# Kernel optimization log

Hardware: AMD Instinct MI355X
Metric: run time of the kernel (lower is better)

## Reference

```python
import jax, jax.numpy as jnp
import numpy as np
from jax import lax

H = 256       # hidden_size (hard-coded via .view(256,1) in source)
V = 10000     # vocab
NOPS = 9      # ops: 0 sum, 1 count, 2 diff, 3 greater, 4 lesser, 5 and, 6 or, 7 assign, 8 reset
COLS = 64
ROWS = 200000
T = 4         # num_time_steps
QLEN = 40
NNUM = 5


def setup_inputs() -> dict:
    key = jax.random.key(0)
    ks = jax.random.split(key, 16)
    s = 0.02
    return {
        'input_question': jax.random.randint(ks[0], (QLEN,), 0, V),
        'question_numbers': jax.random.normal(ks[1], (NNUM,), jnp.float32),
        'left_word_indices': jax.random.randint(ks[2], (NNUM,), 0, QLEN),
        'table': jax.random.normal(ks[3], (ROWS, COLS), jnp.float32),
        # question RNN params
        'E': jax.random.normal(ks[4], (V, H), jnp.float32) * s,
        'Wx': jax.random.normal(ks[5], (H, H), jnp.float32) * s,
        'Wh': jax.random.normal(ks[6], (H, H), jnp.float32) * s,
        'b': jnp.zeros((H,), jnp.float32),
        # selector params
        'W_op': jax.random.normal(ks[7], (H, 2 * H), jnp.float32) * s,
        'op_emb': jax.random.normal(ks[8], (NOPS, H), jnp.float32) * s,
        'W_col': jax.random.normal(ks[9], (H, 2 * H), jnp.float32) * s,
        'col_emb': jax.random.normal(ks[10], (COLS, H), jnp.float32) * s,
        # pivot embeddings U(0)=lesser, U(1)=greater
        'U': jax.random.normal(ks[11], (2, H), jnp.float32) * s,
        # history RNN params
        'W_hc': jax.random.normal(ks[12], (H, 2 * H), jnp.float32) * s,
        'W_hh': jax.random.normal(ks[13], (H, H), jnp.float32) * s,
    }


def reference(input_question, question_numbers, left_word_indices, table,
              E, Wx, Wh, b, W_op, op_emb, W_col, col_emb, U, W_hc, W_hh):
    rows = table.shape[0]
    # ---- question RNN (simple tanh RNN over embedded words) ----
    x = E[input_question]                                  # [Q, H]
    def cell(h, xt):
        hn = jnp.tanh(xt @ Wx + h @ Wh + b)
        return hn, hn
    q, states = lax.scan(cell, jnp.zeros((H,), table.dtype), x)   # q: [H], states: [Q, H]
    Z = states[left_word_indices]                          # z_matrix [N, H]

    # ---- pivots (train mode: soft attention over question numbers) ----
    beta_l = jax.nn.softmax(Z @ U[0])                      # [N]
    beta_g = jax.nn.softmax(Z @ U[1])
    l_pivot = beta_l @ question_numbers                    # scalar
    g_pivot = beta_g @ question_numbers

    row_selects = [jnp.ones((rows,), table.dtype)]
    scalars = [jnp.zeros((), table.dtype)]
    h_hist = jnp.zeros((H,), table.dtype)
    lookup = jnp.zeros(table.shape, table.dtype)

    for t in range(T):
        qh = jnp.concatenate([q, h_hist])                  # [2H]
        a_op = jax.nn.softmax(op_emb @ jnp.tanh(W_op @ qh))    # [NOPS]
        a_col = jax.nn.softmax(col_emb @ jnp.tanh(W_col @ qh)) # [COLS]

        rs1 = row_selects[-1]
        rs2 = row_selects[max(0, len(row_selects) - 2)]
        s1 = scalars[-1]
        s3 = scalars[max(0, len(scalars) - 3)]

        col_val = table @ a_col                            # [R] column-weighted table values
        g_sel = (table > g_pivot).astype(table.dtype) @ a_col  # [R]
        l_sel = (table < l_pivot).astype(table.dtype) @ a_col

        row_select = (a_op[3] * g_sel + a_op[4] * l_sel
                      + a_op[5] * jnp.minimum(rs1, rs2)
                      + a_op[6] * jnp.maximum(rs1, rs2)
                      + a_op[8] * 1.0
                      + (a_op[0] + a_op[1] + a_op[2] + a_op[7]) * rs1)

        scalar = (a_op[0] * (rs1 @ col_val)
                  + a_op[1] * jnp.sum(rs1)
                  + a_op[2] * (s3 - s1))

        lookup = a_op[7] * row_select[:, None] * a_col[None, :]   # [R, C]

        c = jnp.concatenate([a_op @ op_emb, a_col @ col_emb])     # [2H]
        h_hist = jnp.tanh(W_hc @ c + W_hh @ h_hist)

        row_selects.append(row_select)
        scalars.append(scalar)

    return scalars[-1], lookup
```

## Files before the change

### kernel.cpp

```cpp
#include <hip/hip_runtime.h>
#include <math.h>

#define H 256
#define COLSN 64
#define ROWSN 200000
#define T_STEPS 4
#define QLEN 40
#define NNUM 5
#define NOPS 9

#define WS_UBUF   0
#define WS_HBUF   3072
#define WS_XWB    0
#define WS_Q      10240
#define WS_AOP    10496
#define WS_ACOL   10560
#define WS_PIV    10816
#define WS_TICKET 10818
#define WS_PACC8  10824
#define WS_EPOCH  10840
#define WS_ARR    10844
#define WS_MOP    11104
#define WS_MCOL   13408

#define NTBL_TILES  1563
#define NTBL_BLOCKS 782
#define NSEL_BLOCKS 13
#define NM_BLOCKS   72

template<int CTRL>
__device__ __forceinline__ float dpp_add(float x) {
    int xi = __float_as_int(x);
    int yi = __builtin_amdgcn_update_dpp(0, xi, CTRL, 0xF, 0xF, true);
    return x + __int_as_float(yi);
}
#define DPP_XOR1 0xB1
#define DPP_XOR2 0x4E
#define DPP_HMIR 0x141
#define DPP_MIR  0x140

__device__ __forceinline__ float reduce16(float v) {
    v = dpp_add<DPP_XOR1>(v);
    v = dpp_add<DPP_XOR2>(v);
    v = dpp_add<DPP_HMIR>(v);
    v = dpp_add<DPP_MIR>(v);
    return v;
}

__device__ __forceinline__ float fast_tanh(float x) {
    float cx = fminf(15.f, fmaxf(-15.f, x));
    float e = __expf(2.f * cx);
    return __fdividef(e - 1.f, e + 1.f);
}

__device__ __forceinline__ float dot4(float4 a, float4 b) {
    return a.x * b.x + a.y * b.y + a.z * b.z + a.w * b.w;
}

__device__ __forceinline__ float aread(float* p) { return atomicAdd(p, 0.f); }

__device__ __forceinline__ int sw(int i) { return i + ((i >> 4) << 2); }

__global__ __launch_bounds__(256) void k_pre(const int* __restrict__ iq,
        const float* __restrict__ E, const float* __restrict__ Wx,
        const float* __restrict__ b, const float* __restrict__ W_hc,
        const float* __restrict__ op_emb, const float* __restrict__ col_emb,
        float* __restrict__ ws) {
    int blk = blockIdx.x;
    int tid = threadIdx.x;
    if (blk < QLEN) {
        if (blk == 0 && tid < 32) ws[WS_TICKET + tid] = 0.f;
        int word = iq[blk];
        const float* erow = E + (long)word * H;
        float a0 = b[tid], a1 = 0.f, a2 = 0.f, a3 = 0.f;
        #pragma unroll 8
        for (int j = 0; j < H; j += 4) {
            a0 += erow[j + 0] * Wx[(j + 0) * H + tid];
            a1 += erow[j + 1] * Wx[(j + 1) * H + tid];
            a2 += erow[j + 2] * Wx[(j + 2) * H + tid];
            a3 += erow[j + 3] * Wx[(j + 3) * H + tid];
        }
        ws[WS_XWB + blk * H + tid] = (a0 + a1) + (a2 + a3);
    } else {
        __shared__ __attribute__((aligned(16))) float tile[32][268];
        int mb = blk - QLEN;
        int bi = mb / 9;
        int kg = mb % 9;
        int ibase = bi * 32;
        int coff = (kg == 0) ? 0 : H;
        for (int idx = tid; idx < 32 * 64; idx += 256) {
            int r = idx >> 6, c4 = idx & 63;
            float4 v = *(const float4*)&W_hc[(long)(ibase + r) * 2 * H + coff + c4 * 4];
            float* d = &tile[r][c4 * 4];
            d[0] = v.x; d[1] = v.y; d[2] = v.z; d[3] = v.w;
        }
        __syncthreads();
        int l8 = tid & 7;
        int io = tid >> 3;
        int nk = (kg == 0) ? NOPS : 8;
        for (int kk = 0; kk < nk; ++kk) {
            const float* emb;
            int dst;
            if (kg == 0) { emb = op_emb + kk * H;                 dst = WS_MOP + kk * H; }
            else { int c = (kg - 1) * 8 + kk; emb = col_emb + c * H; dst = WS_MCOL + c * H; }
            float s = 0.f;
            const float* ep = emb + l8 * 32;
            const float* tr = &tile[io][l8 * 32];
            #pragma unroll
            for (int ss = 0; ss < 8; ++ss) {
                int q4 = (ss + l8) & 7;
                float4 e4 = *(const float4*)&ep[q4 * 4];
                float4 t4 = *(const float4*)&tr[q4 * 4];
                s += dot4(e4, t4);
            }
            s += __shfl_xor(s, 1);
            s += __shfl_xor(s, 2);
            s += __shfl_xor(s, 4);
            if (l8 == 0) ws[dst + ibase + io] = s;
        }
    }
}

__global__ __launch_bounds__(1024) void k_rnn(const float* __restrict__ Wh,
                      const int* __restrict__ lwi,
                      const float* __restrict__ U, const float* __restrict__ qn,
                      float* __restrict__ ws) {
    __shared__ __attribute__((aligned(16))) float hbuf[2][288];
    __shared__ __attribute__((aligned(16))) float xwb[QLEN][H];
    __shared__ float Z[NNUM][H];
    __shared__ float lg[10];
    int tid = threadIdx.x;
    int g = tid >> 3;
    int p = tid & 7;

    float2 w2[32];
    #pragma unroll
    for (int jj = 0; jj < 32; ++jj)
        w2[jj] = *(const float2*)&Wh[(p * 32 + jj) * H + g * 2];

    {
        const float4* src = (const float4*)&ws[WS_XWB];
        float4* dst = (float4*)&xwb[0][0];
        for (int idx = tid; idx < QLEN * H / 4; idx += 1024) dst[idx] = src[idx];
    }
    if (tid < H) hbuf[0][tid + ((tid >> 5) << 2)] = 0.f;
    __syncthreads();

    int lw0 = lwi[0], lw1 = lwi[1], lw2 = lwi[2], lw3 = lwi[3], lw4 = lwi[4];
    int cur = 0;
    for (int t = 0; t < QLEN; ++t) {
        const float4* hv = (const float4*)&hbuf[cur][p * 36];
        float a0 = 0.f, a1 = 0.f;
        #pragma unroll
        for (int q4 = 0; q4 < 8; ++q4) {
            float4 h4 = hv[q4];
            float2 wa = w2[q4 * 4 + 0];
            float2 wb = w2[q4 * 4 + 1];
            float2 wc = w2[q4 * 4 + 2];
            float2 wd = w2[q4 * 4 + 3];
            a0 += h4.x * wa.x; a1 += h4.x * wa.y;
            a0 += h4.y * wb.x; a1 += h4.y * wb.y;
            a0 += h4.z * wc.x; a1 += h4.z * wc.y;
            a0 += h4.w * wd.x; a1 += h4.w * wd.y;
        }
        a0 = dpp_add<DPP_XOR1>(a0); a0 = dpp_add<DPP_XOR2>(a0); a0 = dpp_add<DPP_HMIR>(a0);
        a1 = dpp_add<DPP_XOR1>(a1); a1 = dpp_add<DPP_XOR2>(a1); a1 = dpp_add<DPP_HMIR>(a1);
        if (p < 2) {
            float s = (p == 0) ? a0 : a1;
            int i = g * 2 + p;
            float hn = fast_tanh(xwb[t][i] + s);
            hbuf[cur ^ 1][i + ((i >> 5) << 2)] = hn;
            if (t == lw0) Z[0][i] = hn;
            if (t == lw1) Z[1][i] = hn;
            if (t == lw2) Z[2][i] = hn;
            if (t == lw3) Z[3][i] = hn;
            if (t == lw4) Z[4][i] = hn;
        }
        __syncthreads();
        cur ^= 1;
    }
    if (tid < H) ws[WS_Q + tid] = hbuf[cur][tid + ((tid >> 5) << 2)];

    int grp = tid >> 5;
    int lane = tid & 31;
    if (grp < 10) {
        int u = grp / 5, n = grp % 5;
        float s = 0.f;
        #pragma unroll
        for (int k = 0; k < 8; ++k) {
            int j = lane + k * 32;
            s += Z[n][j] * U[u * H + j];
        }
        s += __shfl_xor(s, 1);
        s += __shfl_xor(s, 2);
        s += __shfl_xor(s, 4);
        s += __shfl_xor(s, 8);
        s += __shfl_xor(s, 16);
        if (lane == 0) lg[grp] = s;
    }
    __syncthreads();
    if (tid < 2) {
        float m = -1e30f;
        for (int n = 0; n < 5; ++n) m = fmaxf(m, lg[tid * 5 + n]);
        float e[5], s = 0.f;
        for (int n = 0; n < 5; ++n) { e[n] = expf(lg[tid * 5 + n] - m); s += e[n]; }
        float piv = 0.f;
        for (int n = 0; n < 5; ++n) piv += (e[n] / s) * qn[n];
        ws[WS_PIV + (tid == 0 ? 1 : 0)] = piv;
    }
    for (int i = tid; i < 4096; i += 1024) ws[WS_UBUF + i] = 0.f;
}

__global__ __launch_bounds__(256) void k_sel(
        const float* __restrict__ W_op, const float* __restrict__ W_col,
        const float* __restrict__ W_hh, const float* __restrict__ op_emb,
        const float* __restrict__ col_emb, float* __restrict__ ws) {
    const int tid = threadIdx.x;
    const int blk = blockIdx.x;

    if (blk == 0) {
        __shared__ float mopL[NOPS][H];
        __shared__ float mcolL[COLSN][H];
        __shared__ __attribute__((aligned(16))) float uopsw[320];
        __shared__ __attribute__((aligned(16))) float ucolsw[320];
        __shared__ float vhhL[H];
        __shared__ float lgs[80];
        __shared__ float aop_s[16], acol_s[64];

        for (int idx = tid; idx < (NOPS + COLSN) * H; idx += 256) {
            int row = idx >> 8, col = idx & 255;
            if (row < NOPS) mopL[row][col] = ws[WS_MOP + row * H + col];
            else            mcolL[row - NOPS][col] = ws[WS_MCOL + (row - NOPS) * H + col];
        }
        __syncthreads();

        for (int t = 0; t < T_STEPS; ++t) {
            if (tid == 0) {
                while (aread(&ws[WS_ARR + t]) < 11.5f) __builtin_amdgcn_s_sleep(16);
            }
            __syncthreads();
            float uo = aread(&ws[WS_UBUF + t * 768 + tid]);
            float uc = aread(&ws[WS_UBUF + t * 768 + 256 + tid]);
            float vh = aread(&ws[WS_UBUF + t * 768 + 512 + tid]);
            uopsw[sw(tid)] = uo;
            ucolsw[sw(tid)] = uc;
            vhhL[tid] = vh;
            __syncthreads();
            {
                int g = tid >> 4, p = tid & 15;
                int pb = p * 20;
                float4 uc0 = *(const float4*)&ucolsw[pb + 0];
                float4 uc1 = *(const float4*)&ucolsw[pb + 4];
                float4 uc2 = *(const float4*)&ucolsw[pb + 8];
                float4 uc3 = *(const float4*)&ucolsw[pb + 12];
                #pragma unroll
                for (int k = 0; k < 4; ++k) {
                    int o = g + k * 16;
                    const float* row = &col_emb[o * H + p * 16];
                    float4 e0 = *(const float4*)&row[0];
                    float4 e1 = *(const float4*)&row[4];
                    float4 e2 = *(const float4*)&row[8];
                    float4 e3 = *(const float4*)&row[12];
                    float s = dot4(e0, uc0) + dot4(e1, uc1) + dot4(e2, uc2) + dot4(e3, uc3);
                    s = reduce16(s);
                    if (p == 0) lgs[NOPS + o] = s;
                }
                if (g < NOPS) {
                    float4 uo0 = *(const float4*)&uopsw[pb + 0];
                    float4 uo1 = *(const float4*)&uopsw[pb + 4];
                    float4 uo2 = *(const float4*)&uopsw[pb + 8];
                    float4 uo3 = *(const float4*)&uopsw[pb + 12];
                    const float* row = &op_emb[g * H + p * 16];
                    float4 e0 = *(const float4*)&row[0];
                    float4 e1 = *(const float4*)&row[4];
                    float4 e2 = *(const float4*)&row[8];
                    float4 e3 = *(const float4*)&row[12];
                    float s = dot4(e0, uo0) + dot4(e1, uo1) + dot4(e2, uo2) + dot4(e3, uo3);
                    s = reduce16(s);
                    if (p == 0) lgs[g] = s;
                }
            }
            __syncthreads();
            if (tid == 0) {
                float m = -1e30f;
                for (int k = 0; k < NOPS; ++k) m = fmaxf(m, lgs[k]);
                float e[NOPS], s = 0.f;
                for (int k = 0; k < NOPS; ++k) { e[k] = expf(lgs[k] - m); s += e[k]; }
                float inv = 1.f / s;
                for (int k = 0; k < NOPS; ++k) {
                    float a = e[k] * inv;
                    aop_s[k] = a;
                    ws[WS_AOP + t * 16 + k] = a;
                }
            }
            if (tid >= 64 && tid < 128) {
                int lane = tid - 64;
                float v = lgs[NOPS + lane];
                float m = v;
                for (int off = 1; off < 64; off <<= 1) m = fmaxf(m, __shfl_xor(m, off));
                float e = expf(v - m);
                float s = e;
                for (int off = 1; off < 64; off <<= 1) s += __shfl_xor(s, off);
                float a = __fdividef(e, s);
                acol_s[lane] = a;
                ws[WS_ACOL + t * COLSN + lane] = a;
            }
            __syncthreads();
            if (t < T_STEPS - 1) {
                float s = vhhL[tid];
                #pragma unroll
                for (int k = 0; k < NOPS; ++k) s += aop_s[k] * mopL[k][tid];
                #pragma unroll 8
                for (int c = 0; c < COLSN; ++c) s += acol_s[c] * mcolL[c][tid];
                float hn = fast_tanh(s);
                atomicAdd(&ws[WS_HBUF + (t + 1) * 256 + tid], hn);
                __threadfence();
                __syncthreads();
                if (tid == 0) atomicAdd(&ws[WS_EPOCH], 1.f);
            }
        }
    } else {
        __shared__ float wlds[64 * 257];
        __shared__ float hl[H];
        __shared__ float Pl[64];
        __shared__ float pp[4][64];
        const int wb = (blk - 1) * 64;

        for (int idx = tid; idx < 64 * 64; idx += 256) {
            int r = idx >> 6, j4 = idx & 63;
            int o = wb + r;
            const float* src = (o < 256) ? &W_op[(long)o * 2 * H + H]
                             : (o < 512) ? &W_col[(long)(o - 256) * 2 * H + H]
                             : &W_hh[(long)(o - 512) * H];
            float4 v = *(const float4*)&src[j4 * 4];
            float* d = &wlds[r * 257 + j4 * 4];
            d[0] = v.x; d[1] = v.y; d[2] = v.z; d[3] = v.w;
        }
        hl[tid] = ws[WS_Q + tid];
        __syncthreads();
        {
            int r = tid >> 2, c = tid & 3;
            int o = wb + r;
            if (o < 512) {
                const float* src = (o < 256) ? &W_op[(long)o * 2 * H]
                                             : &W_col[(long)(o - 256) * 2 * H];
                const float* qq = &hl[c * 64];
                float s = 0.f;
                #pragma unroll
                for (int k = 0; k < 16; ++k) {
                    float4 w = *(const float4*)&src[c * 64 + k * 4];
                    s += w.x * qq[k*4] + w.y * qq[k*4+1] + w.z * qq[k*4+2] + w.w * qq[k*4+3];
                }
                s += __shfl_xor(s, 1);
                s += __shfl_xor(s, 2);
                if (c == 0) Pl[r] = s;
            } else if (c == 0) Pl[r] = 0.f;
        }
        __syncthreads();

        const int lane = tid & 63;
        const int seg = tid >> 6;
        for (int t = 0; t < T_STEPS; ++t) {
            if (t > 0) {
                if (tid == 0) {
                    while (aread(&ws[WS_EPOCH]) < (float)t - 0.5f) __builtin_amdgcn_s_sleep(16);
                }
                __syncthreads();
                hl[tid] = aread(&ws[WS_HBUF + t * 256 + tid]);
                __syncthreads();
            }
            float s = 0.f;
            if (t > 0) {
                const float* wr = &wlds[lane * 257 + seg * 64];
                const float* hh = &hl[seg * 64];
                #pragma unroll 8
                for (int j = 0; j < 64; ++j) s += wr[j] * hh[j];
            }
            pp[seg][lane] = s;
            __syncthreads();
            if (tid < 64) {
                float sum = pp[0][tid] + pp[1][tid] + pp[2][tid] + pp[3][tid];
                int o = wb + tid;
                float val = (o < 512) ? fast_tanh(Pl[tid] + sum) : sum;
                atomicAdd(&ws[WS_UBUF + t * 768 + o], val);
            }
            __threadfence();
            __syncthreads();
            if (tid == 0) atomicAdd(&ws[WS_ARR + t], 1.f);
            __syncthreads();
        }
    }
}

__global__ __launch_bounds__(512) void k_table(const float* __restrict__ table,
                                               float* __restrict__ ws,
                                               float* __restrict__ out) {
    __shared__ __attribute__((aligned(16))) float4 acT4[4][17];
    __shared__ float aop_l[64];
    __shared__ float rs3s[8][16];
    __shared__ float bred[8][8];
    __shared__ int lastblk;
    const int tid = threadIdx.x;
    const int wid = tid >> 6;
    const int lane = tid & 63;
    const int r16 = lane & 15;
    const int q = lane >> 4;

    if (tid < 64) {
        aop_l[tid] = ws[WS_AOP + tid];
        acT4[tid >> 4][tid & 15] = make_float4(
            ws[WS_ACOL + 0 * COLSN + tid], ws[WS_ACOL + 1 * COLSN + tid],
            ws[WS_ACOL + 2 * COLSN + tid], ws[WS_ACOL + 3 * COLSN + tid]);
    }
    __syncthreads();
    const float gp = ws[WS_PIV + 0];
    const float lp = ws[WS_PIV + 1];
    const float ac3 = acT4[q][r16].w;

    float dacc[4] = {0,0,0,0}, cacc[4] = {0,0,0,0};

    for (int tile = blockIdx.x; tile < NTBL_TILES; tile += NTBL_BLOCKS) {
        long wrow = (long)tile * 128 + wid * 16;
        bool active = wrow < ROWSN;

        float cv[4] = {0,0,0,0}, gs[4] = {0,0,0,0}, ls[4] = {0,0,0,0};
        if (active) {
            const float* src = table + (wrow + r16) * COLSN + q * 16;
            float4 x0 = *(const float4*)&src[0];
            float4 x1 = *(const float4*)&src[4];
            float4 x2 = *(const float4*)&src[8];
            float4 x3 = *(const float4*)&src[12];
            float xs[16] = {x0.x,x0.y,x0.z,x0.w, x1.x,x1.y,x1.z,x1.w,
                            x2.x,x2.y,x2.z,x2.w, x3.x,x3.y,x3.z,x3.w};
            #pragma unroll
            for (int jj = 0; jj < 16; ++jj) {
                float x = xs[jj];
                float4 a4 = acT4[q][jj];
                float gt = (x > gp) ? 1.f : 0.f;
                float lt = (x < lp) ? 1.f : 0.f;
                cv[0] += x * a4.x;  cv[1] += x * a4.y;  cv[2] += x * a4.z;  cv[3] += x * a4.w;
                gs[0] += gt * a4.x; gs[1] += gt * a4.y; gs[2] += gt * a4.z; gs[3] += gt * a4.w;
                ls[0] += lt * a4.x; ls[1] += lt * a4.y; ls[2] += lt * a4.z; ls[3] += lt * a4.w;
            }
        }
        #pragma unroll
        for (int k = 0; k < 4; ++k) {
            cv[k] += __shfl_xor(cv[k], 16); cv[k] += __shfl_xor(cv[k], 32);
            gs[k] += __shfl_xor(gs[k], 16); gs[k] += __shfl_xor(gs[k], 32);
            ls[k] += __shfl_xor(ls[k], 16); ls[k] += __shfl_xor(ls[k], 32);
        }

        float prev1 = 1.f, prev2 = 1.f;
        #pragma unroll
        for (int t = 0; t < 4; ++t) {
            if (active) { dacc[t] += prev1 * cv[t]; cacc[t] += prev1; }
            float cg = aop_l[t*16+3], cl = aop_l[t*16+4], cmn = aop_l[t*16+5];
            float cmx = aop_l[t*16+6], co = aop_l[t*16+8];
            float cid = aop_l[t*16+0] + aop_l[t*16+1] + aop_l[t*16+2] + aop_l[t*16+7];
            float rsn = cg * gs[t] + cl * ls[t] + cmn * fminf(prev1, prev2)
                      + cmx * fmaxf(prev1, prev2) + co + cid * prev1;
            prev2 = prev1; prev1 = rsn;
        }
        if (q == 0 && active) rs3s[wid][r16] = prev1 * aop_l[3*16+7];

        if (active) {
            float* dst = out + 1 + wrow * COLSN;
            #pragma unroll 4
            for (int s = 0; s < 16; ++s)
                dst[(long)s * COLSN + lane] = rs3s[wid][s] * ac3;
        }
    }

    float vals[8];
    #pragma unroll
    for (int t = 0; t < 4; ++t) { vals[t] = dacc[t]; vals[4 + t] = cacc[t]; }
    #pragma unroll
    for (int k = 0; k < 8; ++k) vals[k] = reduce16(vals[k]);
    if (lane == 0) {
        #pragma unroll
        for (int k = 0; k < 8; ++k) bred[wid][k] = vals[k];
    }
    __syncthreads();
    if (tid < 8) {
        float s = 0.f;
        #pragma unroll
        for (int w = 0; w < 8; ++w) s += bred[w][tid];
        atomicAdd(&ws[WS_PACC8 + tid], s);
    }
    __syncthreads();

    if (tid == 0) {
        float old = atomicAdd(&ws[WS_TICKET], 1.0f);
        lastblk = ((int)(old + 0.5f) == NTBL_BLOCKS - 1) ? 1 : 0;
    }
    __syncthreads();
    if (lastblk) {
        if (tid < 8) bred[0][tid] = atomicAdd(&ws[WS_PACC8 + tid], 0.f);
        __syncthreads();
        if (tid == 0) {
            float d0 = bred[0][0], d1 = bred[0][1], d2 = bred[0][2], d3 = bred[0][3];
            float c0 = bred[0][4], c1 = bred[0][5], c2 = bred[0][6], c3 = bred[0][7];
            float s0 = aop_l[0]*d0  + aop_l[1]*c0;
            float s1 = aop_l[16]*d1 + aop_l[17]*c1 + aop_l[18]*(0.f - s0);
            float s2 = aop_l[32]*d2 + aop_l[33]*c2 + aop_l[34]*(0.f - s1);
            float s3 = aop_l[48]*d3 + aop_l[49]*c3 + aop_l[50]*(s0 - s2);
            out[0] = s3;
        }
    }
}

extern "C" void kernel_launch(void* const* d_in, const int* in_sizes, int n_in,
                              void* d_out, int out_size, void* d_ws, size_t ws_size,
                              hipStream_t stream) {
    const int*   iq      = (const int*)  d_in[0];
    const float* qn      = (const float*)d_in[1];
    const int*   lwi     = (const int*)  d_in[2];
    const float* table   = (const float*)d_in[3];
    const float* E       = (const float*)d_in[4];
    const float* Wx      = (const float*)d_in[5];
    const float* Wh      = (const float*)d_in[6];
    const float* b       = (const float*)d_in[7];
    const float* W_op    = (const float*)d_in[8];
    const float* op_emb  = (const float*)d_in[9];
    const float* W_col   = (const float*)d_in[10];
    const float* col_emb = (const float*)d_in[11];
    const float* U       = (const float*)d_in[12];
    const float* W_hc    = (const float*)d_in[13];
    const float* W_hh    = (const float*)d_in[14];
    float* out = (float*)d_out;
    float* ws  = (float*)d_ws;

    hipLaunchKernelGGL(k_pre,  dim3(QLEN + NM_BLOCKS), dim3(256), 0, stream,
                       iq, E, Wx, b, W_hc, op_emb, col_emb, ws);
    hipLaunchKernelGGL(k_rnn,  dim3(1), dim3(1024), 0, stream, Wh, lwi, U, qn, ws);
    hipLaunchKernelGGL(k_sel,  dim3(NSEL_BLOCKS), dim3(256), 0, stream,
                       W_op, W_col, W_hh, op_emb, col_emb, ws);
    hipLaunchKernelGGL(k_table, dim3(NTBL_BLOCKS), dim3(512), 0, stream,
                       table, ws, out);
}
```

Measured before the change: 133.3 us.

## Fuse pre, RNN and selector kernels into one persistent kernel with flag sync

Replaces the separate k_pre, k_rnn and k_sel launches with a tiny zeroing kernel plus one fused 95-block kernel. Inside it, roles are assigned by block index and handed off through global atomic counters (XW done, M done, Q done). The history-RNN step is now computed redundantly in each of the 12 selector blocks from LDS-resident M matrices, which removes the single-block broadcast epoch round-trip. This targets launch gaps and the inter-block serialization per time step, at the cost of spin-wait dependencies that assume all blocks are co-resident, plus redundant compute.

```diff
diff --git a/kernel.cpp b/kernel.cpp
--- a/kernel.cpp
+++ b/kernel.cpp
@@ -10,7 +10,6 @@
 #define NOPS 9
 
 #define WS_UBUF   0
-#define WS_HBUF   3072
 #define WS_XWB    0
 #define WS_Q      10240
 #define WS_AOP    10496
@@ -18,15 +17,19 @@
 #define WS_PIV    10816
 #define WS_TICKET 10818
 #define WS_PACC8  10824
-#define WS_EPOCH  10840
-#define WS_ARR    10844
+#define WS_ARR    10832
+#define WS_XWDONE 10836
+#define WS_MDONE  10837
+#define WS_QDONE  10838
 #define WS_MOP    11104
 #define WS_MCOL   13408
 
 #define NTBL_TILES  1563
 #define NTBL_BLOCKS 782
-#define NSEL_BLOCKS 13
-#define NM_BLOCKS   72
+#define NW 12
+#define NXW 10
+#define NMB 72
+#define NFUSED (NW + 1 + NXW + NMB)
 
 template<int CTRL>
 __device__ __forceinline__ float dpp_add(float x) {
@@ -61,223 +64,122 @@
 
 __device__ __forceinline__ int sw(int i) { return i + ((i >> 4) << 2); }
 
-__global__ __launch_bounds__(256) void k_pre(const int* __restrict__ iq,
-        const float* __restrict__ E, const float* __restrict__ Wx,
-        const float* __restrict__ b, const float* __restrict__ W_hc,
+__global__ void k_zero(float* __restrict__ ws) {
+    int t = threadIdx.x;
+    if (t < 22) ws[WS_TICKET + t] = 0.f;
+}
+
+__global__ __launch_bounds__(1024) void k_fused(
+        const int* __restrict__ iq, const int* __restrict__ lwi,
+        const float* __restrict__ qn, const float* __restrict__ E,
+        const float* __restrict__ Wx, const float* __restrict__ b,
+        const float* __restrict__ Wh, const float* __restrict__ U,
+        const float* __restrict__ W_op, const float* __restrict__ W_col,
+        const float* __restrict__ W_hh, const float* __restrict__ W_hc,
         const float* __restrict__ op_emb, const float* __restrict__ col_emb,
         float* __restrict__ ws) {
-    int blk = blockIdx.x;
-    int tid = threadIdx.x;
-    if (blk < QLEN) {
-        if (blk == 0 && tid < 32) ws[WS_TICKET + tid] = 0.f;
-        int word = iq[blk];
-        const float* erow = E + (long)word * H;
-        float a0 = b[tid], a1 = 0.f, a2 = 0.f, a3 = 0.f;
-        #pragma unroll 8
-        for (int j = 0; j < H; j += 4) {
-            a0 += erow[j + 0] * Wx[(j + 0) * H + tid];
-            a1 += erow[j + 1] * Wx[(j + 1) * H + tid];
-            a2 += erow[j + 2] * Wx[(j + 2) * H + tid];
-            a3 += erow[j + 3] * Wx[(j + 3) * H + tid];
-        }
-        ws[WS_XWB + blk * H + tid] = (a0 + a1) + (a2 + a3);
-    } else {
-        __shared__ __attribute__((aligned(16))) float tile[32][268];
-        int mb = blk - QLEN;
-        int bi = mb / 9;
-        int kg = mb % 9;
-        int ibase = bi * 32;
-        int coff = (kg == 0) ? 0 : H;
-        for (int idx = tid; idx < 32 * 64; idx += 256) {
-            int r = idx >> 6, c4 = idx & 63;
-            float4 v = *(const float4*)&W_hc[(long)(ibase + r) * 2 * H + coff + c4 * 4];
-            float* d = &tile[r][c4 * 4];
-            d[0] = v.x; d[1] = v.y; d[2] = v.z; d[3] = v.w;
-        }
-        __syncthreads();
-        int l8 = tid & 7;
-        int io = tid >> 3;
-        int nk = (kg == 0) ? NOPS : 8;
-        for (int kk = 0; kk < nk; ++kk) {
-            const float* emb;
-            int dst;
-            if (kg == 0) { emb = op_emb + kk * H;                 dst = WS_MOP + kk * H; }
-            else { int c = (kg - 1) * 8 + kk; emb = col_emb + c * H; dst = WS_MCOL + c * H; }
-            float s = 0.f;
-            const float* ep = emb + l8 * 32;
-            const float* tr = &tile[io][l8 * 32];
-            #pragma unroll
-            for (int ss = 0; ss < 8; ++ss) {
-                int q4 = (ss + l8) & 7;
-                float4 e4 = *(const float4*)&ep[q4 * 4];
-                float4 t4 = *(const float4*)&tr[q4 * 4];
-                s += dot4(e4, t4);
-            }
-            s += __shfl_xor(s, 1);
-            s += __shfl_xor(s, 2);
-            s += __shfl_xor(s, 4);
-            if (l8 == 0) ws[dst + ibase + io] = s;
-        }
-    }
-}
-
-__global__ __launch_bounds__(1024) void k_rnn(const float* __restrict__ Wh,
-                      const int* __restrict__ lwi,
-                      const float* __restrict__ U, const float* __restrict__ qn,
-                      float* __restrict__ ws) {
-    __shared__ __attribute__((aligned(16))) float hbuf[2][288];
-    __shared__ __attribute__((aligned(16))) float xwb[QLEN][H];
-    __shared__ float Z[NNUM][H];
-    __shared__ float lg[10];
-    int tid = threadIdx.x;
-    int g = tid >> 3;
-    int p = tid & 7;
-
-    float2 w2[32];
-    #pragma unroll
-    for (int jj = 0; jj < 32; ++jj)
-        w2[jj] = *(const float2*)&Wh[(p * 32 + jj) * H + g * 2];
-
-    {
-        const float4* src = (const float4*)&ws[WS_XWB];
-        float4* dst = (float4*)&xwb[0][0];
-        for (int idx = tid; idx < QLEN * H / 4; idx += 1024) dst[idx] = src[idx];
-    }
-    if (tid < H) hbuf[0][tid + ((tid >> 5) << 2)] = 0.f;
-    __syncthreads();
-
-    int lw0 = lwi[0], lw1 = lwi[1], lw2 = lwi[2], lw3 = lwi[3], lw4 = lwi[4];
-    int cur = 0;
-    for (int t = 0; t < QLEN; ++t) {
-        const float4* hv = (const float4*)&hbuf[cur][p * 36];
-        float a0 = 0.f, a1 = 0.f;
-        #pragma unroll
-        for (int q4 = 0; q4 < 8; ++q4) {
-            float4 h4 = hv[q4];
-            float2 wa = w2[q4 * 4 + 0];
-            float2 wb = w2[q4 * 4 + 1];
-            float2 wc = w2[q4 * 4 + 2];
-            float2 wd = w2[q4 * 4 + 3];
-            a0 += h4.x * wa.x; a1 += h4.x * wa.y;
-            a0 += h4.y * wb.x; a1 += h4.y * wb.y;
-            a0 += h4.z * wc.x; a1 += h4.z * wc.y;
-            a0 += h4.w * wd.x; a1 += h4.w * wd.y;
-        }
-        a0 = dpp_add<DPP_XOR1>(a0); a0 = dpp_add<DPP_XOR2>(a0); a0 = dpp_add<DPP_HMIR>(a0);
-        a1 = dpp_add<DPP_XOR1>(a1); a1 = dpp_add<DPP_XOR2>(a1); a1 = dpp_add<DPP_HMIR>(a1);
-        if (p < 2) {
-            float s = (p == 0) ? a0 : a1;
-            int i = g * 2 + p;
-            float hn = fast_tanh(xwb[t][i] + s);
-            hbuf[cur ^ 1][i + ((i >> 5) << 2)] = hn;
-            if (t == lw0) Z[0][i] = hn;
-            if (t == lw1) Z[1][i] = hn;
-            if (t == lw2) Z[2][i] = hn;
-            if (t == lw3) Z[3][i] = hn;
-            if (t == lw4) Z[4][i] = hn;
-        }
-        __syncthreads();
-        cur ^= 1;
-    }
-    if (tid < H) ws[WS_Q + tid] = hbuf[cur][tid + ((tid >> 5) << 2)];
-
-    int grp = tid >> 5;
-    int lane = tid & 31;
-    if (grp < 10) {
-        int u = grp / 5, n = grp % 5;
-        float s = 0.f;
-        #pragma unroll
-        for (int k = 0; k < 8; ++k) {
-            int j = lane + k * 32;
-            s += Z[n][j] * U[u * H + j];
-        }
-        s += __shfl_xor(s, 1);
-        s += __shfl_xor(s, 2);
-        s += __shfl_xor(s, 4);
-        s += __shfl_xor(s, 8);
-        s += __shfl_xor(s, 16);
-        if (lane == 0) lg[grp] = s;
-    }
-    __syncthreads();
-    if (tid < 2) {
-        float m = -1e30f;
-        for (int n = 0; n < 5; ++n) m = fmaxf(m, lg[tid * 5 + n]);
-        float e[5], s = 0.f;
-        for (int n = 0; n < 5; ++n) { e[n] = expf(lg[tid * 5 + n] - m); s += e[n]; }
-        float piv = 0.f;
-        for (int n = 0; n < 5; ++n) piv += (e[n] / s) * qn[n];
-        ws[WS_PIV + (tid == 0 ? 1 : 0)] = piv;
-    }
-    for (int i = tid; i < 4096; i += 1024) ws[WS_UBUF + i] = 0.f;
-}
-
-__global__ __launch_bounds__(256) void k_sel(
-        const float* __restrict__ W_op, const float* __restrict__ W_col,
-        const float* __restrict__ W_hh, const float* __restrict__ op_emb,
-        const float* __restrict__ col_emb, float* __restrict__ ws) {
+    __shared__ __attribute__((aligned(16))) float smem[36864];
     const int tid = threadIdx.x;
     const int blk = blockIdx.x;
 
-    if (blk == 0) {
-        __shared__ float mopL[NOPS][H];
-        __shared__ float mcolL[COLSN][H];
-        __shared__ __attribute__((aligned(16))) float uopsw[320];
-        __shared__ __attribute__((aligned(16))) float ucolsw[320];
-        __shared__ float vhhL[H];
-        __shared__ float lgs[80];
-        __shared__ float aop_s[16], acol_s[64];
-
-        for (int idx = tid; idx < (NOPS + COLSN) * H; idx += 256) {
-            int row = idx >> 8, col = idx & 255;
-            if (row < NOPS) mopL[row][col] = ws[WS_MOP + row * H + col];
-            else            mcolL[row - NOPS][col] = ws[WS_MCOL + (row - NOPS) * H + col];
-        }
-        __syncthreads();
+    if (blk < NW) {
+        float* wlds  = smem;
+        float* mlds  = smem + 16448;
+        float* hl    = smem + 35136;
+        float* Pl    = smem + 35456;
+        float* uop   = smem + 35520;
+        float* ucol  = smem + 35840;
+        float* vhh   = smem + 36160;
+        float* lgs   = smem + 36416;
+        float* aop_s = smem + 36496;
+        float* acol_s= smem + 36512;
+        const int wb = blk * 64;
+        const int r  = tid >> 4;
+        const int p  = tid & 15;
+        const int pb = p * 20;
+
+        for (int idx = tid; idx < 64 * 64; idx += 1024) {
+            int rr = idx >> 6, j4 = idx & 63;
+            int o = wb + rr;
+            const float* src = (o < 256) ? &W_op[(long)o * 512 + 256]
+                             : (o < 512) ? &W_col[(long)(o - 256) * 512 + 256]
+                             : &W_hh[(long)(o - 512) * 256];
+            float4 v = *(const float4*)&src[j4 * 4];
+            float* d = &wlds[rr * 257 + j4 * 4];
+            d[0] = v.x; d[1] = v.y; d[2] = v.z; d[3] = v.w;
+        }
+        if (tid == 0) while (aread(&ws[WS_MDONE]) < NMB - 0.5f) __builtin_amdgcn_s_sleep(8);
+        __syncthreads();
+        for (int idx = tid; idx < 73 * 256; idx += 1024)
+            mlds[idx] = aread(&ws[WS_MOP + idx]);
+        if (tid == 0) while (aread(&ws[WS_QDONE]) < 0.5f) __builtin_amdgcn_s_sleep(8);
+        __syncthreads();
+        if (tid < 256) hl[sw(tid)] = aread(&ws[WS_Q + tid]);
+        __syncthreads();
+        {
+            int o = wb + r;
+            float s = 0.f;
+            if (o < 512) {
+                const float* row = (o < 256) ? &W_op[(long)o * 512 + p * 16]
+                                             : &W_col[(long)(o - 256) * 512 + p * 16];
+                float4 r0 = *(const float4*)&row[0];
+                float4 r1 = *(const float4*)&row[4];
+                float4 r2 = *(const float4*)&row[8];
+                float4 r3 = *(const float4*)&row[12];
+                const float* qq = &hl[pb];
+                s = dot4(r0, *(const float4*)&qq[0]) + dot4(r1, *(const float4*)&qq[4])
+                  + dot4(r2, *(const float4*)&qq[8]) + dot4(r3, *(const float4*)&qq[12]);
+            }
+            s = reduce16(s);
+            if (p == 0) Pl[r] = s;
+        }
+        __syncthreads();
+        if (tid < 64) {
+            int o = wb + tid;
+            float val = (o < 512) ? fast_tanh(Pl[tid]) : 0.f;
+            atomicExch(&ws[WS_UBUF + 0 * 768 + o], val);
+        }
+        __threadfence();
+        __syncthreads();
+        if (tid == 0) atomicAdd(&ws[WS_ARR + 0], 1.f);
 
         for (int t = 0; t < T_STEPS; ++t) {
-            if (tid == 0) {
-                while (aread(&ws[WS_ARR + t]) < 11.5f) __builtin_amdgcn_s_sleep(16);
-            }
+            if (tid == 0) while (aread(&ws[WS_ARR + t]) < NW - 0.5f) __builtin_amdgcn_s_sleep(1);
             __syncthreads();
-            float uo = aread(&ws[WS_UBUF + t * 768 + tid]);
-            float uc = aread(&ws[WS_UBUF + t * 768 + 256 + tid]);
-            float vh = aread(&ws[WS_UBUF + t * 768 + 512 + tid]);
-            uopsw[sw(tid)] = uo;
-            ucolsw[sw(tid)] = uc;
-            vhhL[tid] = vh;
+            if (tid < 256) {
+                uop[sw(tid)]  = aread(&ws[WS_UBUF + t * 768 + tid]);
+                ucol[sw(tid)] = aread(&ws[WS_UBUF + t * 768 + 256 + tid]);
+                vhh[tid]      = aread(&ws[WS_UBUF + t * 768 + 512 + tid]);
+            }
             __syncthreads();
             {
-                int g = tid >> 4, p = tid & 15;
-                int pb = p * 20;
-                float4 uc0 = *(const float4*)&ucolsw[pb + 0];
-                float4 uc1 = *(const float4*)&ucolsw[pb + 4];
-                float4 uc2 = *(const float4*)&ucolsw[pb + 8];
-                float4 uc3 = *(const float4*)&ucolsw[pb + 12];
-                #pragma unroll
-                for (int k = 0; k < 4; ++k) {
-                    int o = g + k * 16;
-                    const float* row = &col_emb[o * H + p * 16];
-                    float4 e0 = *(const float4*)&row[0];
-                    float4 e1 = *(const float4*)&row[4];
-                    float4 e2 = *(const float4*)&row[8];
-                    float4 e3 = *(const float4*)&row[12];
-                    float s = dot4(e0, uc0) + dot4(e1, uc1) + dot4(e2, uc2) + dot4(e3, uc3);
-                    s = reduce16(s);
-                    if (p == 0) lgs[NOPS + o] = s;
-                }
-                if (g < NOPS) {
-                    float4 uo0 = *(const float4*)&uopsw[pb + 0];
-                    float4 uo1 = *(const float4*)&uopsw[pb + 4];
-                    float4 uo2 = *(const float4*)&uopsw[pb + 8];
-                    float4 uo3 = *(const float4*)&uopsw[pb + 12];
-                    const float* row = &op_emb[g * H + p * 16];
-                    float4 e0 = *(const float4*)&row[0];
-                    float4 e1 = *(const float4*)&row[4];
-                    float4 e2 = *(const float4*)&row[8];
-                    float4 e3 = *(const float4*)&row[12];
-                    float s = dot4(e0, uo0) + dot4(e1, uo1) + dot4(e2, uo2) + dot4(e3, uo3);
-                    s = reduce16(s);
-                    if (p == 0) lgs[g] = s;
+                const float* urow = &ucol[pb];
+                float4 u0 = *(const float4*)&urow[0];
+                float4 u1 = *(const float4*)&urow[4];
+                float4 u2 = *(const float4*)&urow[8];
+                float4 u3 = *(const float4*)&urow[12];
+                const float* erow = &col_emb[r * 256 + p * 16];
+                float4 e0 = *(const float4*)&erow[0];
+                float4 e1 = *(const float4*)&erow[4];
+                float4 e2 = *(const float4*)&erow[8];
+                float4 e3 = *(const float4*)&erow[12];
+                float s = dot4(e0, u0) + dot4(e1, u1) + dot4(e2, u2) + dot4(e3, u3);
+                s = reduce16(s);
+                if (p == 0) lgs[NOPS + r] = s;
+                if (r < NOPS) {
+                    const float* vrow = &uop[pb];
+                    float4 v0 = *(const float4*)&vrow[0];
+                    float4 v1 = *(const float4*)&vrow[4];
+                    float4 v2 = *(const float4*)&vrow[8];
+                    float4 v3 = *(const float4*)&vrow[12];
+                    const float* orow = &op_emb[r * 256 + p * 16];
+                    float4 f0 = *(const float4*)&orow[0];
+                    float4 f1 = *(const float4*)&orow[4];
+                    float4 f2 = *(const float4*)&orow[8];
+                    float4 f3 = *(const float4*)&orow[12];
+                    float so = dot4(f0, v0) + dot4(f1, v1) + dot4(f2, v2) + dot4(f3, v3);
+                    so = reduce16(so);
+                    if (p == 0) lgs[r] = so;
                 }
             }
             __syncthreads();
@@ -290,7 +192,7 @@
                 for (int k = 0; k < NOPS; ++k) {
                     float a = e[k] * inv;
                     aop_s[k] = a;
-                    ws[WS_AOP + t * 16 + k] = a;
+                    if (blk == 0) ws[WS_AOP + t * 16 + k] = a;
                 }
             }
             if (tid >= 64 && tid < 128) {
@@ -303,92 +205,179 @@
                 for (int off = 1; off < 64; off <<= 1) s += __shfl_xor(s, off);
                 float a = __fdividef(e, s);
                 acol_s[lane] = a;
-                ws[WS_ACOL + t * COLSN + lane] = a;
+                if (blk == 0) ws[WS_ACOL + t * COLSN + lane] = a;
             }
             __syncthreads();
             if (t < T_STEPS - 1) {
-                float s = vhhL[tid];
-                #pragma unroll
-                for (int k = 0; k < NOPS; ++k) s += aop_s[k] * mopL[k][tid];
-                #pragma unroll 8
-                for (int c = 0; c < COLSN; ++c) s += acol_s[c] * mcolL[c][tid];
-                float hn = fast_tanh(s);
-                atomicAdd(&ws[WS_HBUF + (t + 1) * 256 + tid], hn);
+                if (tid < 256) {
+                    float s = vhh[tid];
+                    #pragma unroll
+                    for (int k = 0; k < NOPS; ++k) s += aop_s[k] * mlds[k * 256 + tid];
+                    #pragma unroll 8
+                    for (int c = 0; c < COLSN; ++c) s += acol_s[c] * mlds[(NOPS + c) * 256 + tid];
+                    hl[sw(tid)] = fast_tanh(s);
+                }
+                __syncthreads();
+                {
+                    int o = wb + r;
+                    const float* wr = &wlds[r * 257 + p * 16];
+                    float4 w0 = *(const float4*)&wr[0];
+                    float4 w1 = *(const float4*)&wr[4];
+                    float4 w2 = *(const float4*)&wr[8];
+                    float4 w3 = *(const float4*)&wr[12];
+                    const float* hh = &hl[pb];
+                    float s = dot4(w0, *(const float4*)&hh[0]) + dot4(w1, *(const float4*)&hh[4])
+                            + dot4(w2, *(const float4*)&hh[8]) + dot4(w3, *(const float4*)&hh[12]);
+                    s = reduce16(s);
+                    if (p == 0) {
+                        float val = (o < 512) ? fast_tanh(Pl[r] + s) : s;
+                        atomicExch(&ws[WS_UBUF + (t + 1) * 768 + o], val);
+                    }
+                }
                 __threadfence();
                 __syncthreads();
-                if (tid == 0) atomicAdd(&ws[WS_EPOCH], 1.f);
-            }
-        }
+                if (tid == 0) atomicAdd(&ws[WS_ARR + t + 1], 1.f);
+            }
+        }
+    } else if (blk == NW) {
+        float* xwb  = smem;
+        float* hbuf = smem + 10240;
+        float* Z    = smem + 10816;
+        float* lg   = smem + 12096;
+        int g = tid >> 3;
+        int p = tid & 7;
+
+        float2 w2[32];
+        #pragma unroll
+        for (int jj = 0; jj < 32; ++jj)
+            w2[jj] = *(const float2*)&Wh[(p * 32 + jj) * H + g * 2];
+
+        if (tid == 0) while (aread(&ws[WS_XWDONE]) < NXW - 0.5f) __builtin_amdgcn_s_sleep(8);
+        __syncthreads();
+        for (int idx = tid; idx < QLEN * H; idx += 1024) xwb[idx] = aread(&ws[WS_XWB + idx]);
+        if (tid < H) hbuf[0 * 288 + tid + ((tid >> 5) << 2)] = 0.f;
+        __syncthreads();
+
+        int lw0 = lwi[0], lw1 = lwi[1], lw2 = lwi[2], lw3 = lwi[3], lw4 = lwi[4];
+        int cur = 0;
+        for (int t = 0; t < QLEN; ++t) {
+            const float4* hv = (const float4*)&hbuf[cur * 288 + p * 36];
+            float a0 = 0.f, a1 = 0.f;
+            #pragma unroll
+            for (int q4 = 0; q4 < 8; ++q4) {
+                float4 h4 = hv[q4];
+                float2 wa = w2[q4 * 4 + 0];
+                float2 wb2 = w2[q4 * 4 + 1];
+                float2 wc = w2[q4 * 4 + 2];
+                float2 wd = w2[q4 * 4 + 3];
+                a0 += h4.x * wa.x; a1 += h4.x * wa.y;
+                a0 += h4.y * wb2.x; a1 += h4.y * wb2.y;
+                a0 += h4.z * wc.x; a1 += h4.z * wc.y;
+                a0 += h4.w * wd.x; a1 += h4.w * wd.y;
+            }
+            a0 = dpp_add<DPP_XOR1>(a0); a0 = dpp_add<DPP_XOR2>(a0); a0 = dpp_add<DPP_HMIR>(a0);
+            a1 = dpp_add<DPP_XOR1>(a1); a1 = dpp_add<DPP_XOR2>(a1); a1 = dpp_add<DPP_HMIR>(a1);
+            if (p < 2) {
+                float s = (p == 0) ? a0 : a1;
+                int i = g * 2 + p;
+                float hn = fast_tanh(xwb[t * H + i] + s);
+                hbuf[(cur ^ 1) * 288 + i + ((i >> 5) << 2)] = hn;
+                if (t == lw0) Z[0 * 256 + i] = hn;
+                if (t == lw1) Z[1 * 256 + i] = hn;
+                if (t == lw2) Z[2 * 256 + i] = hn;
+                if (t == lw3) Z[3 * 256 + i] = hn;
+                if (t == lw4) Z[4 * 256 + i] = hn;
+            }
+            __syncthreads();
+            cur ^= 1;
+        }
+        if (tid < H) atomicExch(&ws[WS_Q + tid], hbuf[cur * 288 + tid + ((tid >> 5) << 2)]);
+
+        int grp = tid >> 5;
+        int lane = tid & 31;
+        if (grp < 10) {
+            int u = grp / 5, n = grp % 5;
+            float s = 0.f;
+            #pragma unroll
+            for (int k = 0; k < 8; ++k) {
+                int j = lane + k * 32;
+                s += Z[n * 256 + j] * U[u * H + j];
+            }
+            s += __shfl_xor(s, 1);
+            s += __shfl_xor(s, 2);
+            s += __shfl_xor(s, 4);
+            s += __shfl_xor(s, 8);
+            s += __shfl_xor(s, 16);
+            if (lane == 0) lg[grp] = s;
+        }
+        __syncthreads();
+        if (tid < 2) {
+            float m = -1e30f;
+            for (int n = 0; n < 5; ++n) m = fmaxf(m, lg[tid * 5 + n]);
+            float e[5], s = 0.f;
+            for (int n = 0; n < 5; ++n) { e[n] = expf(lg[tid * 5 + n] - m); s += e[n]; }
+            float piv = 0.f;
+            for (int n = 0; n < 5; ++n) piv += (e[n] / s) * qn[n];
+            ws[WS_PIV + (tid == 0 ? 1 : 0)] = piv;
+        }
+        __threadfence();
+        __syncthreads();
+        if (tid == 0) atomicAdd(&ws[WS_QDONE], 1.f);
+    } else if (blk < NW + 1 + NXW) {
+        int widx = (blk - NW - 1) * 4 + (tid >> 8);
+        int i = tid & 255;
+        int word = iq[widx];
+        const float* erow = E + (long)word * H;
+        float a0 = b[i], a1 = 0.f, a2 = 0.f, a3 = 0.f;
+        #pragma unroll 8
+        for (int j = 0; j < H; j += 4) {
+            a0 += erow[j + 0] * Wx[(j + 0) * H + i];
+            a1 += erow[j + 1] * Wx[(j + 1) * H + i];
+            a2 += erow[j + 2] * Wx[(j + 2) * H + i];
+            a3 += erow[j + 3] * Wx[(j + 3) * H + i];
+        }
+        atomicExch(&ws[WS_XWB + widx * H + i], (a0 + a1) + (a2 + a3));
+        __threadfence();
+        __syncthreads();
+        if (tid == 0) atomicAdd(&ws[WS_XWDONE], 1.f);
     } else {
-        __shared__ float wlds[64 * 257];
-        __shared__ float hl[H];
-        __shared__ float Pl[64];
-        __shared__ float pp[4][64];
-        const int wb = (blk - 1) * 64;
-
-        for (int idx = tid; idx < 64 * 64; idx += 256) {
-            int r = idx >> 6, j4 = idx & 63;
-            int o = wb + r;
-            const float* src = (o < 256) ? &W_op[(long)o * 2 * H + H]
-                             : (o < 512) ? &W_col[(long)(o - 256) * 2 * H + H]
-                             : &W_hh[(long)(o - 512) * H];
-            float4 v = *(const float4*)&src[j4 * 4];
-            float* d = &wlds[r * 257 + j4 * 4];
+        float* tile = smem;
+        int mb = blk - NW - 1 - NXW;
+        int bi = mb / 9;
+        int kg = mb % 9;
+        int ibase = bi * 32;
+        int coff = (kg == 0) ? 0 : H;
+        for (int idx = tid; idx < 32 * 64; idx += 1024) {
+            int rr = idx >> 6, c4 = idx & 63;
+            float4 v = *(const float4*)&W_hc[(long)(ibase + rr) * 512 + coff + c4 * 4];
+            float* d = &tile[rr * 268 + c4 * 4];
             d[0] = v.x; d[1] = v.y; d[2] = v.z; d[3] = v.w;
         }
-        hl[tid] = ws[WS_Q + tid];
-        __syncthreads();
-        {
-            int r = tid >> 2, c = tid & 3;
-            int o = wb + r;
-            if (o < 512) {
-                const float* src = (o < 256) ? &W_op[(long)o * 2 * H]
-                                             : &W_col[(long)(o - 256) * 2 * H];
-                const float* qq = &hl[c * 64];
-                float s = 0.f;
-                #pragma unroll
-                for (int k = 0; k < 16; ++k) {
-                    float4 w = *(const float4*)&src[c * 64 + k * 4];
-                    s += w.x * qq[k*4] + w.y * qq[k*4+1] + w.z * qq[k*4+2] + w.w * qq[k*4+3];
-                }
-                s += __shfl_xor(s, 1);
-                s += __shfl_xor(s, 2);
-                if (c == 0) Pl[r] = s;
-            } else if (c == 0) Pl[r] = 0.f;
-        }
-        __syncthreads();
-
-        const int lane = tid & 63;
-        const int seg = tid >> 6;
-        for (int t = 0; t < T_STEPS; ++t) {
-            if (t > 0) {
-                if (tid == 0) {
-                    while (aread(&ws[WS_EPOCH]) < (float)t - 0.5f) __builtin_amdgcn_s_sleep(16);
-                }
-                __syncthreads();
-                hl[tid] = aread(&ws[WS_HBUF + t * 256 + tid]);
-                __syncthreads();
-            }
+        __syncthreads();
+        int io = tid >> 5;
+        int l32 = tid & 31;
+        int nk = (kg == 0) ? NOPS : 8;
+        for (int kk = 0; kk < nk; ++kk) {
+            const float* emb;
+            int dst;
+            if (kg == 0) { emb = op_emb + kk * H; dst = WS_MOP + kk * H; }
+            else { int c = (kg - 1) * 8 + kk; emb = col_emb + c * H; dst = WS_MCOL + c * H; }
             float s = 0.f;
-            if (t > 0) {
-                const float* wr = &wlds[lane * 257 + seg * 64];
-                const float* hh = &hl[seg * 64];
-                #pragma unroll 8
-                for (int j = 0; j < 64; ++j) s += wr[j] * hh[j];
-            }
-            pp[seg][lane] = s;
-            __syncthreads();
-            if (tid < 64) {
-                float sum = pp[0][tid] + pp[1][tid] + pp[2][tid] + pp[3][tid];
-                int o = wb + tid;
-                float val = (o < 512) ? fast_tanh(Pl[tid] + sum) : sum;
-                atomicAdd(&ws[WS_UBUF + t * 768 + o], val);
-            }
-            __threadfence();
-            __syncthreads();
-            if (tid == 0) atomicAdd(&ws[WS_ARR + t], 1.f);
-            __syncthreads();
-        }
+            #pragma unroll
+            for (int q8 = 0; q8 < 8; ++q8) {
+                int q = (q8 + l32) & 7;
+                s += tile[io * 268 + l32 * 8 + q] * emb[l32 * 8 + q];
+            }
+            s += __shfl_xor(s, 1);
+            s += __shfl_xor(s, 2);
+            s += __shfl_xor(s, 4);
+            s += __shfl_xor(s, 8);
+            s += __shfl_xor(s, 16);
+            if (l32 == 0) atomicExch(&ws[dst + ibase + io], s);
+        }
+        __threadfence();
+        __syncthreads();
+        if (tid == 0) atomicAdd(&ws[WS_MDONE], 1.f);
     }
 }
 
@@ -530,11 +519,10 @@
     float* out = (float*)d_out;
     float* ws  = (float*)d_ws;
 
-    hipLaunchKernelGGL(k_pre,  dim3(QLEN + NM_BLOCKS), dim3(256), 0, stream,
-                       iq, E, Wx, b, W_hc, op_emb, col_emb, ws);
-    hipLaunchKernelGGL(k_rnn,  dim3(1), dim3(1024), 0, stream, Wh, lwi, U, qn, ws);
-    hipLaunchKernelGGL(k_sel,  dim3(NSEL_BLOCKS), dim3(256), 0, stream,
-                       W_op, W_col, W_hh, op_emb, col_emb, ws);
+    hipLaunchKernelGGL(k_zero, dim3(1), dim3(64), 0, stream, ws);
+    hipLaunchKernelGGL(k_fused, dim3(NFUSED), dim3(1024), 0, stream,
+                       iq, lwi, qn, E, Wx, b, Wh, U, W_op, W_col, W_hh,
+                       W_hc, op_emb, col_emb, ws);
     hipLaunchKernelGGL(k_table, dim3(NTBL_BLOCKS), dim3(512), 0, stream,
                        table, ws, out);
 }
```

After: 143.8 us. 7.8% more time.
